# Performance work log

Hardware: AMD Instinct MI355X
Metric: run time of the kernel (lower is better)

Reference implementation:

```python
import jax, jax.numpy as jnp
import numpy as np

B, S, D, H = 2, 2048, 2048, 16
DK = D // H
THETA = 10000.0


def setup_inputs() -> dict:
    key = jax.random.key(0)
    ks = jax.random.split(key, 5)
    scale = 0.02
    return {
        "x": jax.random.normal(ks[0], (B, S, D), dtype=jnp.float32),
        "W_Q": jax.random.normal(ks[1], (D, D), dtype=jnp.float32) * scale,
        "W_K": jax.random.normal(ks[2], (D, D), dtype=jnp.float32) * scale,
        "W_V": jax.random.normal(ks[3], (D, D), dtype=jnp.float32) * scale,
        "W_O": jax.random.normal(ks[4], (D, D), dtype=jnp.float32) * scale,
        "token_positions": jnp.arange(S, dtype=jnp.int32),
    }


def _rope(x, pos):
    # x: [B, S, H, DK]; pos: [S]. Interleaved-pair rotation (cs336 RoPE).
    half = DK // 2
    inv_freq = THETA ** (-(jnp.arange(half, dtype=jnp.float32) / half))  # [half]
    ang = pos.astype(jnp.float32)[:, None] * inv_freq[None, :]           # [S, half]
    cos = jnp.cos(ang)[None, :, None, :]                                 # [1,S,1,half]
    sin = jnp.sin(ang)[None, :, None, :]
    x1, x2 = x[..., ::2], x[..., 1::2]
    r1 = x1 * cos - x2 * sin
    r2 = x1 * sin + x2 * cos
    return jnp.stack([r1, r2], axis=-1).reshape(x.shape)


def reference(x, W_Q, W_K, W_V, W_O, token_positions):
    # QKV projections (Linear with no bias: y = x @ W^T)
    Q = (x @ W_Q.T).reshape(B, S, H, DK)
    K = (x @ W_K.T).reshape(B, S, H, DK)
    V = (x @ W_V.T).reshape(B, S, H, DK)
    Q = _rope(Q, token_positions)
    K = _rope(K, token_positions)
    scores = jnp.einsum("bqhd,bkhd->bhqk", Q, K) / jnp.sqrt(jnp.float32(DK))
    causal = jnp.tril(jnp.ones((S, S), dtype=bool))  # True = attend
    scores = jnp.where(causal[None, None], scores, -jnp.inf)
    attn = jax.nn.softmax(scores, axis=-1)
    out = jnp.einsum("bhqk,bkhd->bqhd", attn, V).reshape(B, S, D)
    return out @ W_O.T
```

## Files before the change

kernel.cpp:

```cpp
#include <hip/hip_runtime.h>
#include <hip/hip_bf16.h>
#include <cstdint>
#include <cstddef>

#define B_ 2
#define S_ 2048
#define D_ 2048
#define H_ 16
#define DK_ 128
#define M_ (B_*S_)

typedef __attribute__((ext_vector_type(8))) __bf16 bf16x8;
typedef __attribute__((ext_vector_type(4))) float f32x4;

__device__ __forceinline__ unsigned short f2bf(float f) {
  union { float f; unsigned int u; } v; v.f = f;
  unsigned int r = (v.u + 0x7fffu + ((v.u >> 16) & 1u)) >> 16;
  return (unsigned short)r;
}
__device__ __forceinline__ float bf2f(unsigned short b) {
  union { unsigned int u; float f; } v; v.u = ((unsigned int)b) << 16;
  return v.f;
}

__device__ __forceinline__ void gld16(const void* g, void* l) {
  __builtin_amdgcn_global_load_lds(
      (const __attribute__((address_space(1))) unsigned int*)g,
      (__attribute__((address_space(3))) unsigned int*)l, 16, 0, 0);
}

__global__ void cvt_bf16(const float* __restrict__ src, unsigned short* __restrict__ dst, int n) {
  int i = (blockIdx.x * blockDim.x + threadIdx.x) * 4;
  if (i + 3 < n) {
    float4 v = *(const float4*)(src + i);
    dst[i+0] = f2bf(v.x); dst[i+1] = f2bf(v.y);
    dst[i+2] = f2bf(v.z); dst[i+3] = f2bf(v.w);
  }
}

template<int WRITE_BF16>
__global__ __launch_bounds__(256) void gemm_bt(const unsigned short* __restrict__ A,
                                               const unsigned short* __restrict__ W0,
                                               const unsigned short* __restrict__ W1,
                                               const unsigned short* __restrict__ W2,
                                               void* __restrict__ C0, void* __restrict__ C1,
                                               void* __restrict__ C2,
                                               int M, int N, int K) {
  __shared__ unsigned short sA[128 * 32];
  __shared__ unsigned short sB[128 * 32];
  const int z = blockIdx.z;
  const unsigned short* Bt = (z == 0) ? W0 : (z == 1) ? W1 : W2;
  void* Cout = (z == 0) ? C0 : (z == 1) ? C1 : C2;

  const int tid  = threadIdx.x;
  const int lane = tid & 63;
  const int wid  = tid >> 6;
  const int wm = wid >> 1, wn = wid & 1;
  const int quad = lane >> 4, l16 = lane & 15;
  const int bm = blockIdx.y * 128, bn = blockIdx.x * 128;
  const int srow = lane >> 2;
  const int scol = (lane & 3) * 8;

  f32x4 acc[4][4];
  #pragma unroll
  for (int i = 0; i < 4; ++i)
    #pragma unroll
    for (int j = 0; j < 4; ++j)
      acc[i][j] = (f32x4){0.f, 0.f, 0.f, 0.f};

  for (int k0 = 0; k0 < K; k0 += 32) {
    __syncthreads();
    #pragma unroll
    for (int p = 0; p < 2; ++p) {
      int row = p * 64 + wid * 16;
      gld16(A  + (size_t)(bm + row + srow) * K + k0 + scol, sA + row * 32);
      gld16(Bt + (size_t)(bn + row + srow) * K + k0 + scol, sB + row * 32);
    }
    __syncthreads();

    bf16x8 af[4], bfr[4];
    #pragma unroll
    for (int i = 0; i < 4; ++i)
      af[i] = *(const bf16x8*)(sA + (wm * 64 + i * 16 + l16) * 32 + quad * 8);
    #pragma unroll
    for (int j = 0; j < 4; ++j)
      bfr[j] = *(const bf16x8*)(sB + (wn * 64 + j * 16 + l16) * 32 + quad * 8);
    #pragma unroll
    for (int i = 0; i < 4; ++i)
      #pragma unroll
      for (int j = 0; j < 4; ++j)
        acc[i][j] = __builtin_amdgcn_mfma_f32_16x16x32_bf16(af[i], bfr[j], acc[i][j], 0, 0, 0);
  }

  #pragma unroll
  for (int i = 0; i < 4; ++i) {
    int row = bm + wm * 64 + i * 16 + quad * 4;
    #pragma unroll
    for (int j = 0; j < 4; ++j) {
      int col = bn + wn * 64 + j * 16 + l16;
      #pragma unroll
      for (int r = 0; r < 4; ++r) {
        if (WRITE_BF16)
          ((unsigned short*)Cout)[(size_t)(row + r) * N + col] = f2bf(acc[i][j][r]);
        else
          ((float*)Cout)[(size_t)(row + r) * N + col] = acc[i][j][r];
      }
    }
  }
}

__global__ void rope_kernel(unsigned short* __restrict__ Q, unsigned short* __restrict__ K,
                            const int* __restrict__ pos) {
  int idx = blockIdx.x * blockDim.x + threadIdx.x;
  int i = idx & 63;
  int h = (idx >> 6) & (H_ - 1);
  int s = (idx >> 10) & (S_ - 1);
  int b = idx >> 21;
  float p = (float)pos[s];
  float inv = expf(-(float)i * (9.210340371976184f / 64.0f));
  float ang = p * inv;
  float sn, cs;
  sincosf(ang, &sn, &cs);
  size_t base = (((size_t)b * S_ + s) * D_) + (size_t)h * DK_ + 2 * i;
  float x1 = bf2f(Q[base]), x2 = bf2f(Q[base + 1]);
  Q[base]     = f2bf(x1 * cs - x2 * sn);
  Q[base + 1] = f2bf(x1 * sn + x2 * cs);
  x1 = bf2f(K[base]); x2 = bf2f(K[base + 1]);
  K[base]     = f2bf(x1 * cs - x2 * sn);
  K[base + 1] = f2bf(x1 * sn + x2 * cs);
}

__global__ __launch_bounds__(256) void transpose_bf16(const unsigned short* __restrict__ src,
                                                      unsigned short* __restrict__ dst) {
  __shared__ unsigned short sT[64 * 64];
  const int b = blockIdx.y;
  const int tx = blockIdx.x & 31, ty = blockIdx.x >> 5;
  const size_t base = (size_t)b * 2048 * 2048;
  const int m0 = ty * 64, c0 = tx * 64;
  const int tid = threadIdx.x;
  #pragma unroll
  for (int c = 0; c < 2; ++c) {
    int idx = tid + c * 256;
    int row = idx >> 3;
    int chk = idx & 7;
    uint4 v = *(const uint4*)(src + base + (size_t)(m0 + row) * 2048 + c0 + chk * 8);
    *(uint4*)(sT + row * 64 + ((chk ^ (row & 7)) * 8)) = v;
  }
  __syncthreads();
  #pragma unroll
  for (int c = 0; c < 2; ++c) {
    int idx = tid + c * 256;
    int orow = idx >> 3;
    int ocol = (idx & 7) * 8;
    unsigned short tmp[8];
    #pragma unroll
    for (int j = 0; j < 8; ++j) {
      int lr = ocol + j;
      int lc = orow;
      tmp[j] = sT[lr * 64 + (((lc >> 3) ^ (lr & 7)) * 8) + (lc & 7)];
    }
    *(uint4*)(dst + base + (size_t)(c0 + orow) * 2048 + m0 + ocol) = *(const uint4*)tmp;
  }
}

__global__ __launch_bounds__(256, 2) void flash_attn(const unsigned short* __restrict__ Q,
                                                     const unsigned short* __restrict__ K,
                                                     const unsigned short* __restrict__ VT,
                                                     unsigned short* __restrict__ O) {
  __shared__ unsigned short sK[2][64 * 128];
  __shared__ unsigned short sVT[2][128 * 64];
  __shared__ unsigned short sP[4][16 * 72];

  const int tid = threadIdx.x, lane = tid & 63, wid = tid >> 6;
  const int quad = lane >> 4, l16 = lane & 15;
  const int qi = 31 - (blockIdx.x & 31);
  const int bh = blockIdx.x >> 5;
  const int h = bh & (H_ - 1), b = bh >> 4;
  const int qw = qi * 64 + wid * 16;
  const size_t qkbase = ((size_t)b * S_) * D_ + (size_t)h * DK_;
  const unsigned short* Qg = Q + qkbase;
  const unsigned short* Kg = K + qkbase;
  const unsigned short* VTg = VT + (size_t)bh * DK_ * S_;
  unsigned short* Og = O + qkbase;
  unsigned short* sPw = sP[wid];

  const int kKey4 = lane >> 4;
  const int kPhys = lane & 15;
  const int vFeat8 = lane >> 3;
  const int vPhys = lane & 7;

  bf16x8 qf[4];
  #pragma unroll
  for (int kk = 0; kk < 4; ++kk)
    qf[kk] = *(const bf16x8*)(Qg + (size_t)(qw + l16) * D_ + kk * 32 + quad * 8);

  union { unsigned short u[8]; bf16x8 v; } onesu;
  #pragma unroll
  for (int j = 0; j < 8; ++j) onesu.u[j] = 0x3F80;
  const bf16x8 ones = onesu.v;

  f32x4 Oacc[8];
  #pragma unroll
  for (int d = 0; d < 8; ++d) Oacc[d] = (f32x4){0.f, 0.f, 0.f, 0.f};
  f32x4 l_acc = (f32x4){0.f, 0.f, 0.f, 0.f};
  const float scale = 0.08838834764831845f;

  const int nkb = qi + 1;

  auto stage = [&](int kb) {
    const int k0 = kb * 64;
    unsigned short* bK = sK[kb & 1];
    unsigned short* bV = sVT[kb & 1];
    #pragma unroll
    for (int p = 0; p < 4; ++p) {
      int issue = wid * 4 + p;
      int key = issue * 4 + kKey4;
      int logiK = (kPhys & 8) | ((kPhys ^ (key & 7)) & 7);
      gld16(Kg + (size_t)(k0 + key) * D_ + logiK * 8, bK + issue * 512);
      int feat = issue * 8 + vFeat8;
      int logiV = vPhys ^ (feat & 7);
      gld16(VTg + (size_t)feat * S_ + k0 + logiV * 8, bV + issue * 512);
    }
  };

  stage(0);

  for (int kb = 0; kb < nkb; ++kb) {
    __syncthreads();
    if (kb + 1 < nkb) stage(kb + 1);

    const unsigned short* bK = sK[kb & 1];
    const unsigned short* bV = sVT[kb & 1];
    const int k0 = kb * 64;

    f32x4 sc[4];
    #pragma unroll
    for (int t = 0; t < 4; ++t) sc[t] = (f32x4){0.f,0.f,0.f,0.f};
    #pragma unroll
    for (int kk = 0; kk < 4; ++kk) {
      const int chunk = kk * 4 + quad;
      #pragma unroll
      for (int t = 0; t < 4; ++t) {
        const int key = t * 16 + l16;
        const int phys = (chunk & 8) | ((chunk ^ (key & 7)) & 7);
        bf16x8 kf = *(const bf16x8*)(bK + key * 128 + phys * 8);
        sc[t] = __builtin_amdgcn_mfma_f32_16x16x32_bf16(qf[kk], kf, sc[t], 0, 0, 0);
      }
    }

    const bool diag = (kb == nkb - 1);
    #pragma unroll
    for (int r = 0; r < 4; ++r) {
      const int rowg = qw + quad * 4 + r;
      #pragma unroll
      for (int t = 0; t < 4; ++t) {
        float v = sc[t][r] * scale;
        if (diag && (k0 + t * 16 + l16 > rowg)) v = -1e30f;
        sPw[(quad * 4 + r) * 72 + t * 16 + l16] = f2bf(__expf(v));
      }
    }

    #pragma unroll
    for (int t2 = 0; t2 < 2; ++t2) {
      bf16x8 pf = *(const bf16x8*)(sPw + l16 * 72 + t2 * 32 + quad * 8);
      l_acc = __builtin_amdgcn_mfma_f32_16x16x32_bf16(pf, ones, l_acc, 0, 0, 0);
      #pragma unroll
      for (int d = 0; d < 8; ++d) {
        const int feat = d * 16 + l16;
        const int phys = (t2 * 4 + quad) ^ (feat & 7);
        bf16x8 vf = *(const bf16x8*)(bV + feat * 64 + phys * 8);
        Oacc[d] = __builtin_amdgcn_mfma_f32_16x16x32_bf16(pf, vf, Oacc[d], 0, 0, 0);
      }
    }
  }

  #pragma unroll
  for (int d = 0; d < 8; ++d)
    #pragma unroll
    for (int r = 0; r < 4; ++r) {
      int rowg = qw + quad * 4 + r;
      Og[(size_t)rowg * D_ + d * 16 + l16] = f2bf(Oacc[d][r] / l_acc[r]);
    }
}

extern "C" void kernel_launch(void* const* d_in, const int* in_sizes, int n_in,
                              void* d_out, int out_size, void* d_ws, size_t ws_size,
                              hipStream_t stream) {
  const float* x  = (const float*)d_in[0];
  const float* Wq = (const float*)d_in[1];
  const float* Wk = (const float*)d_in[2];
  const float* Wv = (const float*)d_in[3];
  const float* Wo = (const float*)d_in[4];
  const int*  pos = (const int*)d_in[5];
  float* out = (float*)d_out;

  char* ws = (char*)d_ws;
  size_t off = 0;
  auto alloc = [&](size_t bytes) { void* p = ws + off; off += (bytes + 255) & ~255ULL; return p; };
  const size_t nx = (size_t)M_ * D_;
  const size_t nw = (size_t)D_ * D_;
  unsigned short* xb  = (unsigned short*)alloc(nx * 2);
  unsigned short* wqb = (unsigned short*)alloc(nw * 2);
  unsigned short* wkb = (unsigned short*)alloc(nw * 2);
  unsigned short* wvb = (unsigned short*)alloc(nw * 2);
  unsigned short* wob = (unsigned short*)alloc(nw * 2);
  unsigned short* Qb  = (unsigned short*)alloc(nx * 2);
  unsigned short* Kb  = (unsigned short*)alloc(nx * 2);
  unsigned short* Vb  = (unsigned short*)alloc(nx * 2);
  unsigned short* AOb = xb;
  unsigned short* VTb = wqb;

  hipLaunchKernelGGL(cvt_bf16, dim3(nx / 1024), dim3(256), 0, stream, x,  xb,  (int)nx);
  hipLaunchKernelGGL(cvt_bf16, dim3(nw / 1024), dim3(256), 0, stream, Wq, wqb, (int)nw);
  hipLaunchKernelGGL(cvt_bf16, dim3(nw / 1024), dim3(256), 0, stream, Wk, wkb, (int)nw);
  hipLaunchKernelGGL(cvt_bf16, dim3(nw / 1024), dim3(256), 0, stream, Wv, wvb, (int)nw);
  hipLaunchKernelGGL(cvt_bf16, dim3(nw / 1024), dim3(256), 0, stream, Wo, wob, (int)nw);

  hipLaunchKernelGGL((gemm_bt<1>), dim3(D_ / 128, M_ / 128, 3), dim3(256), 0, stream,
                     xb, wqb, wkb, wvb, (void*)Qb, (void*)Kb, (void*)Vb, M_, D_, D_);

  hipLaunchKernelGGL(rope_kernel, dim3((B_ * S_ * H_ * 64) / 256), dim3(256), 0, stream, Qb, Kb, pos);

  hipLaunchKernelGGL(transpose_bf16, dim3(1024, 2), dim3(256), 0, stream, Vb, VTb);

  hipLaunchKernelGGL(flash_attn, dim3(B_ * H_ * (S_ / 64)), dim3(256), 0, stream, Qb, Kb, VTb, AOb);

  hipLaunchKernelGGL((gemm_bt<0>), dim3(D_ / 128, M_ / 128, 1), dim3(256), 0, stream,
                     AOb, wob, wob, wob, (void*)out, (void*)out, (void*)out, M_, D_, D_);
}
```

Before: 473.6 us.

## Use 32x32 MFMA tiles and 128-row query blocks in flash attention

Flash attention now processes 128 query rows per block, with 32 rows per warp, using 32x32x16 bf16 MFMAs instead of 16x16x32. Each K/V tile staged in LDS is reused by twice as many query rows, and the larger MFMA shape needs fewer operand loads per flop. Warps skip key blocks that lie entirely above their causal diagonal, and the P buffer gets an XOR swizzle. The trade-offs are half as many blocks, more causal imbalance within a block, and larger accumulator register use.

```diff
diff --git a/kernel.cpp b/kernel.cpp
--- a/kernel.cpp
+++ b/kernel.cpp
@@ -12,6 +12,7 @@
 
 typedef __attribute__((ext_vector_type(8))) __bf16 bf16x8;
 typedef __attribute__((ext_vector_type(4))) float f32x4;
+typedef __attribute__((ext_vector_type(16))) float f32x16;
 
 __device__ __forceinline__ unsigned short f2bf(float f) {
   union { float f; unsigned int u; } v; v.f = f;
@@ -169,14 +170,14 @@
                                                      unsigned short* __restrict__ O) {
   __shared__ unsigned short sK[2][64 * 128];
   __shared__ unsigned short sVT[2][128 * 64];
-  __shared__ unsigned short sP[4][16 * 72];
+  __shared__ unsigned short sP[4][32 * 64];
 
   const int tid = threadIdx.x, lane = tid & 63, wid = tid >> 6;
-  const int quad = lane >> 4, l16 = lane & 15;
-  const int qi = 31 - (blockIdx.x & 31);
-  const int bh = blockIdx.x >> 5;
+  const int half = lane >> 5, l32 = lane & 31;
+  const int qi = 15 - (blockIdx.x & 15);
+  const int bh = blockIdx.x >> 4;
   const int h = bh & (H_ - 1), b = bh >> 4;
-  const int qw = qi * 64 + wid * 16;
+  const int qw = qi * 128 + wid * 32;
   const size_t qkbase = ((size_t)b * S_) * D_ + (size_t)h * DK_;
   const unsigned short* Qg = Q + qkbase;
   const unsigned short* Kg = K + qkbase;
@@ -184,28 +185,32 @@
   unsigned short* Og = O + qkbase;
   unsigned short* sPw = sP[wid];
 
-  const int kKey4 = lane >> 4;
-  const int kPhys = lane & 15;
-  const int vFeat8 = lane >> 3;
-  const int vPhys = lane & 7;
-
-  bf16x8 qf[4];
-  #pragma unroll
-  for (int kk = 0; kk < 4; ++kk)
-    qf[kk] = *(const bf16x8*)(Qg + (size_t)(qw + l16) * D_ + kk * 32 + quad * 8);
+  const int kKeySub = lane >> 4;
+  const int kPhys   = lane & 15;
+  const int vFeatSub = lane >> 3;
+  const int vPhys    = lane & 7;
+
+  bf16x8 qf[8];
+  #pragma unroll
+  for (int ks = 0; ks < 8; ++ks)
+    qf[ks] = *(const bf16x8*)(Qg + (size_t)(qw + l32) * D_ + ks * 16 + half * 8);
 
   union { unsigned short u[8]; bf16x8 v; } onesu;
   #pragma unroll
   for (int j = 0; j < 8; ++j) onesu.u[j] = 0x3F80;
   const bf16x8 ones = onesu.v;
 
-  f32x4 Oacc[8];
-  #pragma unroll
-  for (int d = 0; d < 8; ++d) Oacc[d] = (f32x4){0.f, 0.f, 0.f, 0.f};
-  f32x4 l_acc = (f32x4){0.f, 0.f, 0.f, 0.f};
+  f32x16 Oacc[4];
+  #pragma unroll
+  for (int ft = 0; ft < 4; ++ft)
+    #pragma unroll
+    for (int r = 0; r < 16; ++r) Oacc[ft][r] = 0.f;
+  f32x16 l_acc;
+  #pragma unroll
+  for (int r = 0; r < 16; ++r) l_acc[r] = 0.f;
   const float scale = 0.08838834764831845f;
 
-  const int nkb = qi + 1;
+  const int nkb = 2 * (qi + 1);
 
   auto stage = [&](int kb) {
     const int k0 = kb * 64;
@@ -214,10 +219,10 @@
     #pragma unroll
     for (int p = 0; p < 4; ++p) {
       int issue = wid * 4 + p;
-      int key = issue * 4 + kKey4;
-      int logiK = (kPhys & 8) | ((kPhys ^ (key & 7)) & 7);
+      int key = issue * 4 + kKeySub;
+      int logiK = (kPhys & 8) | ((kPhys ^ key) & 7);
       gld16(Kg + (size_t)(k0 + key) * D_ + logiK * 8, bK + issue * 512);
-      int feat = issue * 8 + vFeat8;
+      int feat = issue * 8 + vFeatSub;
       int logiV = vPhys ^ (feat & 7);
       gld16(VTg + (size_t)feat * S_ + k0 + logiV * 8, bV + issue * 512);
     }
@@ -229,58 +234,67 @@
     __syncthreads();
     if (kb + 1 < nkb) stage(kb + 1);
 
+    const int k0 = kb * 64;
+    if (k0 > qw + 31) continue;
+
     const unsigned short* bK = sK[kb & 1];
     const unsigned short* bV = sVT[kb & 1];
-    const int k0 = kb * 64;
-
-    f32x4 sc[4];
-    #pragma unroll
-    for (int t = 0; t < 4; ++t) sc[t] = (f32x4){0.f,0.f,0.f,0.f};
-    #pragma unroll
-    for (int kk = 0; kk < 4; ++kk) {
-      const int chunk = kk * 4 + quad;
-      #pragma unroll
-      for (int t = 0; t < 4; ++t) {
-        const int key = t * 16 + l16;
-        const int phys = (chunk & 8) | ((chunk ^ (key & 7)) & 7);
+
+    f32x16 sc[2];
+    #pragma unroll
+    for (int t = 0; t < 2; ++t)
+      #pragma unroll
+      for (int r = 0; r < 16; ++r) sc[t][r] = 0.f;
+    #pragma unroll
+    for (int ks = 0; ks < 8; ++ks) {
+      const int logi = ks * 2 + half;
+      #pragma unroll
+      for (int t = 0; t < 2; ++t) {
+        const int key = t * 32 + l32;
+        const int phys = (logi & 8) | ((logi ^ key) & 7);
         bf16x8 kf = *(const bf16x8*)(bK + key * 128 + phys * 8);
-        sc[t] = __builtin_amdgcn_mfma_f32_16x16x32_bf16(qf[kk], kf, sc[t], 0, 0, 0);
+        sc[t] = __builtin_amdgcn_mfma_f32_32x32x16_bf16(qf[ks], kf, sc[t], 0, 0, 0);
       }
     }
 
-    const bool diag = (kb == nkb - 1);
-    #pragma unroll
-    for (int r = 0; r < 4; ++r) {
-      const int rowg = qw + quad * 4 + r;
-      #pragma unroll
-      for (int t = 0; t < 4; ++t) {
+    const bool diag = (k0 + 63 > qw);
+    #pragma unroll
+    for (int t = 0; t < 2; ++t) {
+      const int col = t * 32 + l32;
+      const int keyg = k0 + col;
+      #pragma unroll
+      for (int r = 0; r < 16; ++r) {
+        const int rl = (r & 3) + 8 * (r >> 2) + 4 * half;
         float v = sc[t][r] * scale;
-        if (diag && (k0 + t * 16 + l16 > rowg)) v = -1e30f;
-        sPw[(quad * 4 + r) * 72 + t * 16 + l16] = f2bf(__expf(v));
+        if (diag && (keyg > qw + rl)) v = -1e30f;
+        sPw[rl * 64 + (((col >> 3) ^ (rl & 7)) * 8) + (col & 7)] = f2bf(__expf(v));
       }
     }
 
     #pragma unroll
-    for (int t2 = 0; t2 < 2; ++t2) {
-      bf16x8 pf = *(const bf16x8*)(sPw + l16 * 72 + t2 * 32 + quad * 8);
-      l_acc = __builtin_amdgcn_mfma_f32_16x16x32_bf16(pf, ones, l_acc, 0, 0, 0);
-      #pragma unroll
-      for (int d = 0; d < 8; ++d) {
-        const int feat = d * 16 + l16;
-        const int phys = (t2 * 4 + quad) ^ (feat & 7);
+    for (int ksp = 0; ksp < 4; ++ksp) {
+      const int logi = ksp * 2 + half;
+      bf16x8 pf = *(const bf16x8*)(sPw + l32 * 64 + ((logi ^ (l32 & 7)) * 8));
+      l_acc = __builtin_amdgcn_mfma_f32_32x32x16_bf16(pf, ones, l_acc, 0, 0, 0);
+      #pragma unroll
+      for (int ft = 0; ft < 4; ++ft) {
+        const int feat = ft * 32 + l32;
+        const int phys = logi ^ (feat & 7);
         bf16x8 vf = *(const bf16x8*)(bV + feat * 64 + phys * 8);
-        Oacc[d] = __builtin_amdgcn_mfma_f32_16x16x32_bf16(pf, vf, Oacc[d], 0, 0, 0);
+        Oacc[ft] = __builtin_amdgcn_mfma_f32_32x32x16_bf16(pf, vf, Oacc[ft], 0, 0, 0);
       }
     }
   }
 
   #pragma unroll
-  for (int d = 0; d < 8; ++d)
-    #pragma unroll
-    for (int r = 0; r < 4; ++r) {
-      int rowg = qw + quad * 4 + r;
-      Og[(size_t)rowg * D_ + d * 16 + l16] = f2bf(Oacc[d][r] / l_acc[r]);
-    }
+  for (int ft = 0; ft < 4; ++ft) {
+    const int feat = ft * 32 + l32;
+    #pragma unroll
+    for (int r = 0; r < 16; ++r) {
+      const int rl = (r & 3) + 8 * (r >> 2) + 4 * half;
+      Og[(size_t)(qw + rl) * D_ + feat] = f2bf(Oacc[ft][r] / l_acc[r]);
+    }
+  }
 }
 
 extern "C" void kernel_launch(void* const* d_in, const int* in_sizes, int n_in,
@@ -323,7 +337,7 @@
 
   hipLaunchKernelGGL(transpose_bf16, dim3(1024, 2), dim3(256), 0, stream, Vb, VTb);
 
-  hipLaunchKernelGGL(flash_attn, dim3(B_ * H_ * (S_ / 64)), dim3(256), 0, stream, Qb, Kb, VTb, AOb);
+  hipLaunchKernelGGL(flash_attn, dim3(B_ * H_ * (S_ / 128)), dim3(256), 0, stream, Qb, Kb, VTb, AOb);
 
   hipLaunchKernelGGL((gemm_bt<0>), dim3(D_ / 128, M_ / 128, 1), dim3(256), 0, stream,
                      AOb, wob, wob, wob, (void*)out, (void*)out, (void*)out, M_, D_, D_);
```

Result: faster. 459.9 us (-2.9%).
